# Kernel tuning notes

Hardware: AMD Instinct MI355X
Metric: run time of the kernel (lower is better)

## Reference

```python
import jax, jax.numpy as jnp
import numpy as np

B, N, F, K = 4, 512, 128, 32
GAMMA = 10.0          # RBF width parameter
CUTOFF = 5.0          # RBF center range [0, CUTOFF]
LOG2 = 0.6931471805599453
EPS = 1e-12           # keeps sqrt grad finite on the (masked-out) diagonal


def ssp(x):
    # shifted softplus: ln(0.5*e^x + 0.5) = softplus(x) - ln 2
    return jax.nn.softplus(x) - LOG2


def setup_inputs() -> dict:
    key = jax.random.key(0)
    ks = jax.random.split(key, 8)
    coordinates = jax.random.normal(ks[0], (B, N, 3), dtype=jnp.float32) * 3.0
    atom_emb = jax.random.normal(ks[1], (B, N, F), dtype=jnp.float32)
    rbf_centers = jnp.linspace(0.0, CUTOFF, K, dtype=jnp.float32)
    # cfconv filter-generator dense layers
    w1 = jax.random.normal(ks[2], (K, F), dtype=jnp.float32) / np.float32(np.sqrt(K))
    b1 = jnp.zeros((F,), dtype=jnp.float32)
    w2 = jax.random.normal(ks[3], (F, F), dtype=jnp.float32) / np.float32(np.sqrt(F))
    b2 = jnp.zeros((F,), dtype=jnp.float32)
    # self.W linear (nn.Linear stores weight as [out, in])
    Ww = jax.random.normal(ks[4], (F, F), dtype=jnp.float32) / np.float32(np.sqrt(F))
    Wb = jnp.zeros((F,), dtype=jnp.float32)
    return {"coordinates": coordinates, "atom_emb": atom_emb,
            "rbf_centers": rbf_centers, "w1": w1, "b1": b1,
            "w2": w2, "b2": b2, "Ww": Ww, "Wb": Wb}


def reference(coordinates, atom_emb, rbf_centers, w1, b1, w2, b2, Ww, Wb):
    n = coordinates.shape[-2]
    # pairwise distances [B, N, N]
    diff = coordinates[:, :, None, :] - coordinates[:, None, :, :]
    d = jnp.sqrt(jnp.sum(diff * diff, axis=-1) + EPS)
    # Gaussian RBF expansion [B, N, N, K]
    rbf = jnp.exp(-GAMMA * (d[..., None] - rbf_centers) ** 2)
    # filter generator: Dense -> SSP -> Dense -> SSP  => W [B, N, N, F]
    Wf = ssp(jnp.einsum('bnmk,kf->bnmf', rbf, w1) + b1)
    Wf = ssp(jnp.einsum('bnmf,fg->bnmg', Wf, w2) + b2)
    # zero the diagonal (no self-interaction)
    mask = (1.0 - jnp.eye(n, dtype=Wf.dtype))[None, :, :, None]
    Wf = Wf * mask
    # x = self.W(atom_emb)
    x = atom_emb @ Ww.T + Wb
    # per-channel weighted neighbor aggregation
    x = jnp.einsum('bnmf,bmf->bnf', Wf, x)
    return atom_emb + x
```

## Files before the change

kernel.cpp:

```cpp
#include <hip/hip_runtime.h>
#include <hip/hip_bf16.h>

#define B_ 4
#define N_ 512
#define F_ 128
#define K_ 32
#define TD 512
#define DMAX 6.5f
#define XWB (B_ * N_ / 2)

typedef __attribute__((ext_vector_type(4))) float f32x4;

__device__ __forceinline__ unsigned cvt_pk_bf16(float a, float b) {
  unsigned r;
  asm("v_cvt_pk_bf16_f32 %0, %1, %2" : "=v"(r) : "v"(a), "v"(b));
  return r;
}
__device__ __forceinline__ unsigned short f2bf1(float a) {
  return (unsigned short)cvt_pk_bf16(a, a);
}
__device__ __forceinline__ float exp2_hw(float x) {
  float r; asm("v_exp_f32 %0, %1" : "=v"(r) : "v"(x)); return r;
}
__device__ __forceinline__ float log2_hw(float x) {
  float r; asm("v_log_f32 %0, %1" : "=v"(r) : "v"(x)); return r;
}
__device__ __forceinline__ float lo16f(unsigned w) {
  return __builtin_bit_cast(float, w << 16);
}
__device__ __forceinline__ float hi16f(unsigned w) {
  return __builtin_bit_cast(float, w & 0xffff0000u);
}

__device__ __forceinline__ float sspb(float u) {
  float e = exp2_hw(__builtin_fabsf(u) * -1.4426950408889634f);
  float l = log2_hw(fmaf(e, 0.5f, 0.5f));
  return fmaf(l, 0.6931471805599453f, fmaxf(u, 0.f));
}

__launch_bounds__(256)
__global__ void prep_kernel(const float* __restrict__ emb, const float* __restrict__ Ww,
                            const float* __restrict__ Wb,
                            const float* __restrict__ w1, const float* __restrict__ b1,
                            const float* __restrict__ w2, const float* __restrict__ b2,
                            unsigned short* __restrict__ xbf, unsigned* __restrict__ tab2) {
  __shared__ float erow[2][F_];
  __shared__ float rbf_s[2][K_];
  __shared__ float h1s[2][F_];
  __shared__ float fs[2][F_];

  if (blockIdx.x < XWB) {
    const int r0 = blockIdx.x * 2;
    const int half = threadIdx.x >> 7, f = threadIdx.x & 127;
    erow[half][f] = emb[(r0 + half) * F_ + f];
    __syncthreads();
    const float4* w4 = (const float4*)(Ww + f * F_);
    const float* er = erow[half];
    float acc = 0.f;
#pragma unroll 8
    for (int g4 = 0; g4 < F_ / 4; ++g4) {
      float4 wv = w4[g4];
      acc = fmaf(er[g4 * 4 + 0], wv.x, acc);
      acc = fmaf(er[g4 * 4 + 1], wv.y, acc);
      acc = fmaf(er[g4 * 4 + 2], wv.z, acc);
      acc = fmaf(er[g4 * 4 + 3], wv.w, acc);
    }
    xbf[(r0 + half) * F_ + f] = f2bf1(acc + Wb[f]);
  } else {
    const int i = blockIdx.x - XWB;
    const int sl = threadIdx.x >> 7, f = threadIdx.x & 127;
    const float d = (float)(i + sl) * (DMAX / (float)(TD - 1));
    if (f < K_) {
      float t = d - (float)f * (5.0f / 31.0f);
      rbf_s[sl][f] = exp2_hw(t * t * -14.426950408889634f);
    }
    __syncthreads();
    float a1 = b1[f];
#pragma unroll 8
    for (int k = 0; k < K_; ++k) a1 = fmaf(rbf_s[sl][k], w1[k * F_ + f], a1);
    h1s[sl][f] = sspb(a1);
    __syncthreads();
    float a2 = b2[f];
#pragma unroll 8
    for (int g = 0; g < F_; ++g) a2 = fmaf(h1s[sl][g], w2[g * F_ + f], a2);
    fs[sl][f] = sspb(a2);
    __syncthreads();
    if (sl == 0)
      tab2[i * F_ + f] = cvt_pk_bf16(fs[0][f], fs[1][f] - fs[0][f]);
  }
}

__launch_bounds__(256, 8)
__global__ void agg_kernel(const float* __restrict__ coords, const float* __restrict__ emb,
                           const unsigned short* __restrict__ xbf,
                           const unsigned* __restrict__ tab2,
                           float* __restrict__ out) {
  __shared__ float tvr[N_];
  __shared__ float ctv[N_ + 1];
  __shared__ unsigned cid[N_ + 1];
  __shared__ unsigned cnt_s;
  __shared__ float part[16][F_ + 4];

  const int blk = blockIdx.x;
  const int b = blk >> 9, n = blk & 511;
  const int tid = threadIdx.x;
  const int lane = tid & 63;

  const float cx = coords[(b * N_ + n) * 3 + 0];
  const float cy = coords[(b * N_ + n) * 3 + 1];
  const float cz = coords[(b * N_ + n) * 3 + 2];

  for (int m = tid; m < N_; m += 256) {
    const float* cm = coords + (b * N_ + m) * 3;
    float dx = cm[0] - cx, dy = cm[1] - cy, dz = cm[2] - cz;
    float d = sqrtf(fmaf(dx, dx, fmaf(dy, dy, fmaf(dz, dz, 1e-12f))));
    tvr[m] = d * ((float)(TD - 1) / DMAX);
  }
  __syncthreads();

  const float TKEEP = 6.0f * ((float)(TD - 1) / DMAX);
  if (tid < 64) {
    unsigned base = 0;
#pragma unroll 1
    for (int chunk = 0; chunk < N_ / 64; ++chunk) {
      int m = chunk * 64 + lane;
      float tv = tvr[m];
      bool keep = (tv < TKEEP) && (m != n);
      unsigned long long msk = __ballot(keep);
      unsigned pos = base + (unsigned)__popcll(msk & ((1ull << lane) - 1ull));
      if (keep) { ctv[pos] = tv; cid[pos] = (unsigned)m; }
      base += (unsigned)__popcll(msk);
    }
    if (lane == 0) {
      cnt_s = base;
      ctv[base] = 0.f;
      cid[base] = 0u;
    }
  }
  __syncthreads();
  const int cnt = (int)cnt_s;

  const int mg = tid >> 4;
  const int f0 = (tid & 15) * 8;
  const unsigned short* xp = xbf + b * N_ * F_ + f0;

  f32x4 acc0 = {0.f, 0.f, 0.f, 0.f};
  f32x4 acc1 = {0.f, 0.f, 0.f, 0.f};

  int k = mg;
  int idx = (k < cnt) ? k : cnt;
  float tv = ctv[idx];
  unsigned id = cid[idx];
  int ii = (int)tv;
  float fr = tv - (float)ii;
  const uint4* tp = (const uint4*)(tab2 + ii * F_ + f0);
  uint4 ta = tp[0], tb = tp[1];
  uint4 xv = *(const uint4*)(xp + id * F_);

#pragma unroll 1
  while (k < cnt) {
    int kn = k + 16;
    int idxn = (kn < cnt) ? kn : cnt;
    float tvn = ctv[idxn];
    unsigned idn = cid[idxn];
    int iin = (int)tvn;
    float frn = tvn - (float)iin;
    const uint4* tpn = (const uint4*)(tab2 + iin * F_ + f0);
    uint4 tan = tpn[0], tbn = tpn[1];
    uint4 xvn = *(const uint4*)(xp + idn * F_);

    float v;
    v = fmaf(fr, hi16f(ta.x), lo16f(ta.x));
    acc0[0] = fmaf(v, lo16f(xv.x), acc0[0]);
    v = fmaf(fr, hi16f(ta.y), lo16f(ta.y));
    acc0[1] = fmaf(v, hi16f(xv.x), acc0[1]);
    v = fmaf(fr, hi16f(ta.z), lo16f(ta.z));
    acc0[2] = fmaf(v, lo16f(xv.y), acc0[2]);
    v = fmaf(fr, hi16f(ta.w), lo16f(ta.w));
    acc0[3] = fmaf(v, hi16f(xv.y), acc0[3]);
    v = fmaf(fr, hi16f(tb.x), lo16f(tb.x));
    acc1[0] = fmaf(v, lo16f(xv.z), acc1[0]);
    v = fmaf(fr, hi16f(tb.y), lo16f(tb.y));
    acc1[1] = fmaf(v, hi16f(xv.z), acc1[1]);
    v = fmaf(fr, hi16f(tb.z), lo16f(tb.z));
    acc1[2] = fmaf(v, lo16f(xv.w), acc1[2]);
    v = fmaf(fr, hi16f(tb.w), lo16f(tb.w));
    acc1[3] = fmaf(v, hi16f(xv.w), acc1[3]);

    k = kn; fr = frn; ta = tan; tb = tbn; xv = xvn;
  }

  *(f32x4*)&part[mg][f0] = acc0;
  *(f32x4*)&part[mg][f0 + 4] = acc1;
  __syncthreads();

  if (tid < F_) {
    float s = 0.f;
#pragma unroll
    for (int g = 0; g < 16; ++g) s += part[g][tid];
    int o = (b * N_ + n) * F_ + tid;
    out[o] = emb[o] + s;
  }
}

extern "C" void kernel_launch(void* const* d_in, const int* in_sizes, int n_in,
                              void* d_out, int out_size, void* d_ws, size_t ws_size,
                              hipStream_t stream) {
  const float* coords = (const float*)d_in[0];
  const float* emb    = (const float*)d_in[1];
  const float* w1 = (const float*)d_in[3];
  const float* b1 = (const float*)d_in[4];
  const float* w2 = (const float*)d_in[5];
  const float* b2 = (const float*)d_in[6];
  const float* Ww = (const float*)d_in[7];
  const float* Wb = (const float*)d_in[8];
  float* out = (float*)d_out;

  unsigned short* xbf = (unsigned short*)d_ws;
  unsigned* tab2 = (unsigned*)(xbf + B_ * N_ * F_);

  hipLaunchKernelGGL(prep_kernel, dim3(XWB + TD - 1), dim3(256), 0, stream,
                     emb, Ww, Wb, w1, b1, w2, b2, xbf, tab2);
  hipLaunchKernelGGL(agg_kernel, dim3(B_ * N_), dim3(256), 0, stream,
                     coords, emb, xbf, tab2, out);
}
```

Before: 41.36 us.

## Split neighbor range across two blocks per atom with atomic accumulation

```diff
diff --git a/kernel.cpp b/kernel.cpp
--- a/kernel.cpp
+++ b/kernel.cpp
@@ -8,6 +8,7 @@
 #define TD 512
 #define DMAX 6.5f
 #define XWB (B_ * N_ / 2)
+#define HM 256
 
 typedef __attribute__((ext_vector_type(4))) float f32x4;
 
@@ -43,7 +44,8 @@
                             const float* __restrict__ Wb,
                             const float* __restrict__ w1, const float* __restrict__ b1,
                             const float* __restrict__ w2, const float* __restrict__ b2,
-                            unsigned short* __restrict__ xbf, unsigned* __restrict__ tab2) {
+                            unsigned short* __restrict__ xbf, unsigned* __restrict__ tab2,
+                            float* __restrict__ out) {
   __shared__ float erow[2][F_];
   __shared__ float rbf_s[2][K_];
   __shared__ float h1s[2][F_];
@@ -52,7 +54,9 @@
   if (blockIdx.x < XWB) {
     const int r0 = blockIdx.x * 2;
     const int half = threadIdx.x >> 7, f = threadIdx.x & 127;
-    erow[half][f] = emb[(r0 + half) * F_ + f];
+    float ev = emb[(r0 + half) * F_ + f];
+    erow[half][f] = ev;
+    out[(r0 + half) * F_ + f] = ev;
     __syncthreads();
     const float4* w4 = (const float4*)(Ww + f * F_);
     const float* er = erow[half];
@@ -91,18 +95,21 @@
 }
 
 __launch_bounds__(256, 8)
-__global__ void agg_kernel(const float* __restrict__ coords, const float* __restrict__ emb,
+__global__ void agg_kernel(const float* __restrict__ coords,
                            const unsigned short* __restrict__ xbf,
                            const unsigned* __restrict__ tab2,
                            float* __restrict__ out) {
-  __shared__ float tvr[N_];
-  __shared__ float ctv[N_ + 1];
-  __shared__ unsigned cid[N_ + 1];
+  __shared__ float tvr[HM];
+  __shared__ float ctv[HM + 1];
+  __shared__ unsigned cid[HM + 1];
   __shared__ unsigned cnt_s;
   __shared__ float part[16][F_ + 4];
 
   const int blk = blockIdx.x;
-  const int b = blk >> 9, n = blk & 511;
+  const int b = blk >> 10;
+  const int r = blk & 1023;
+  const int n = r >> 1;
+  const int m0 = (r & 1) * HM;
   const int tid = threadIdx.x;
   const int lane = tid & 63;
 
@@ -110,25 +117,26 @@
   const float cy = coords[(b * N_ + n) * 3 + 1];
   const float cz = coords[(b * N_ + n) * 3 + 2];
 
-  for (int m = tid; m < N_; m += 256) {
+  {
+    const int m = m0 + tid;
     const float* cm = coords + (b * N_ + m) * 3;
     float dx = cm[0] - cx, dy = cm[1] - cy, dz = cm[2] - cz;
     float d = sqrtf(fmaf(dx, dx, fmaf(dy, dy, fmaf(dz, dz, 1e-12f))));
-    tvr[m] = d * ((float)(TD - 1) / DMAX);
+    tvr[tid] = d * ((float)(TD - 1) / DMAX);
   }
   __syncthreads();
 
   const float TKEEP = 6.0f * ((float)(TD - 1) / DMAX);
   if (tid < 64) {
     unsigned base = 0;
-#pragma unroll 1
-    for (int chunk = 0; chunk < N_ / 64; ++chunk) {
-      int m = chunk * 64 + lane;
-      float tv = tvr[m];
-      bool keep = (tv < TKEEP) && (m != n);
+#pragma unroll
+    for (int chunk = 0; chunk < HM / 64; ++chunk) {
+      int ml = chunk * 64 + lane;
+      float tv = tvr[ml];
+      bool keep = (tv < TKEEP) && (m0 + ml != n);
       unsigned long long msk = __ballot(keep);
       unsigned pos = base + (unsigned)__popcll(msk & ((1ull << lane) - 1ull));
-      if (keep) { ctv[pos] = tv; cid[pos] = (unsigned)m; }
+      if (keep) { ctv[pos] = tv; cid[pos] = (unsigned)(m0 + ml); }
       base += (unsigned)__popcll(msk);
     }
     if (lane == 0) {
@@ -198,8 +206,7 @@
     float s = 0.f;
 #pragma unroll
     for (int g = 0; g < 16; ++g) s += part[g][tid];
-    int o = (b * N_ + n) * F_ + tid;
-    out[o] = emb[o] + s;
+    unsafeAtomicAdd(&out[(b * N_ + n) * F_ + tid], s);
   }
 }
 
@@ -220,7 +227,7 @@
   unsigned* tab2 = (unsigned*)(xbf + B_ * N_ * F_);
 
   hipLaunchKernelGGL(prep_kernel, dim3(XWB + TD - 1), dim3(256), 0, stream,
-                     emb, Ww, Wb, w1, b1, w2, b2, xbf, tab2);
-  hipLaunchKernelGGL(agg_kernel, dim3(B_ * N_), dim3(256), 0, stream,
-                     coords, emb, xbf, tab2, out);
-}
+                     emb, Ww, Wb, w1, b1, w2, b2, xbf, tab2, out);
+  hipLaunchKernelGGL(agg_kernel, dim3(B_ * N_ * 2), dim3(256), 0, stream,
+                     coords, xbf, tab2, out);
+}
```

After: 40.03 us. 1.03x faster.
